# Kernel optimization log

Measured on AMD Instinct MI355X. Metric: run time of the kernel, lower is better.

Reference implementation:

```python
import jax, jax.numpy as jnp
import numpy as np

# EntNet entity-memory update (Henaff et al. 2017), per selected entity i:
#   g_i      = sigmoid(s . h_i + s . w_i)                       (gate)
#   h~_i     = relu(h_i @ U^T + w_i @ V^T + s @ W^T)            (candidate)
#   h_i      = l2_normalize(h_i + g_i * h~_i)
# The original TF code loops over `indices` in Python; since each index touches a
# distinct entity slot, the updates are independent and we vectorize with a single
# gather over the entity axis and a scatter (.at[].set) back.

def setup_inputs() -> dict:
    key = jax.random.key(0)
    ks = jax.random.split(key, 6)
    B, N, D, K = 32, 1024, 1024, 512
    return {
        "encoded_sents": jax.random.normal(ks[0], (B, D), jnp.float32),
        "hiddens": jax.random.normal(ks[1], (B, N, D), jnp.float32),
        "keys": jax.random.normal(ks[2], (B, N, D), jnp.float32),
        "U": jax.random.normal(ks[3], (D, D), jnp.float32),
        "V": jax.random.normal(ks[4], (D, D), jnp.float32),
        "W": jax.random.normal(ks[5], (D, D), jnp.float32),
        "indices": jnp.arange(K, dtype=jnp.int64),
    }

def reference(encoded_sents, hiddens, keys, U, V, W, indices):
    EPS = 1e-12
    h = hiddens[:, indices, :]                     # [B,K,D] gather selected entities
    w = keys[:, indices, :]                        # [B,K,D]
    s = encoded_sents                              # [B,D]
    # gate: sigmoid(s.h_i + s.w_i) -> [B,K]
    g = jax.nn.sigmoid(jnp.einsum('bd,bkd->bk', s, h + w))
    # candidate: relu(h U^T + w V^T + s W^T) -> [B,K,D]
    h_tilde = jax.nn.relu(
        jnp.einsum('bkd,ed->bke', h, U)
        + jnp.einsum('bkd,ed->bke', w, V)
        + (s @ W.T)[:, None, :]
    )
    h_new = h + g[..., None] * h_tilde
    # tf.math.l2_normalize: x * rsqrt(max(sum(x^2), eps))
    h_new = h_new * jax.lax.rsqrt(jnp.maximum(jnp.sum(h_new * h_new, axis=-1, keepdims=True), EPS))
    # scatter updated entities back
    return hiddens.at[:, indices, :].set(h_new)
```

## Files before the change

kernel.cpp:

```cpp
#include <hip/hip_runtime.h>

constexpr int Bb = 32;
constexpr int Nn = 1024;
constexpr int Dd = 1024;
constexpr int Kk = 512;
constexpr int Mm = Bb * Kk;
constexpr int KD = 2 * Dd;

using bf16x8 = __bf16 __attribute__((ext_vector_type(8)));
using f32x4  = float __attribute__((ext_vector_type(4)));

constexpr size_t WS_ABF  = 0;
constexpr size_t WS_BBF  = (size_t)Mm * KD * 2;
constexpr size_t WS_G    = WS_BBF + (size_t)Nn * KD * 2;
constexpr size_t WS_SW   = WS_G + Mm * sizeof(float);
constexpr size_t WS_RN   = WS_SW + Bb * Nn * sizeof(float);
constexpr size_t WS_MASK = WS_RN + Mm * sizeof(float);

__global__ void mask_kernel(const int* __restrict__ idx, int* __restrict__ mask) {
  int t = threadIdx.x;
  mask[t] = 0;
  __syncthreads();
  if (t < Kk) mask[idx[t]] = 1;
}

__global__ void copy_kernel(const float* __restrict__ hiddens,
                            const int* __restrict__ mask,
                            float* __restrict__ out) {
  int bid = blockIdx.x;
  int n = bid & (Nn - 1);
  if (mask[n]) return;
  size_t base = (size_t)bid * Dd + threadIdx.x * 4;
  *(f32x4*)(out + base) = *(const f32x4*)(hiddens + base);
}

__global__ void prep_b_kernel(const float* __restrict__ U,
                              const float* __restrict__ V,
                              __bf16* __restrict__ Bbf) {
  int t = blockIdx.x * 256 + threadIdx.x;
  int e = t >> 8;
  int c = (t & 255) << 3;
  const float* src = (c < Dd) ? (U + (size_t)e * Dd + c)
                              : (V + (size_t)e * Dd + (c - Dd));
  f32x4 f0 = *(const f32x4*)src;
  f32x4 f1 = *(const f32x4*)(src + 4);
  bf16x8 v;
  v[0] = (__bf16)f0[0]; v[1] = (__bf16)f0[1]; v[2] = (__bf16)f0[2]; v[3] = (__bf16)f0[3];
  v[4] = (__bf16)f1[0]; v[5] = (__bf16)f1[1]; v[6] = (__bf16)f1[2]; v[7] = (__bf16)f1[3];
  *(bf16x8*)(Bbf + (size_t)e * KD + c) = v;
}

__global__ void sw_kernel(const float* __restrict__ s,
                          const float* __restrict__ W,
                          float* __restrict__ sW) {
  int e = blockIdx.x * 4 + (threadIdx.x >> 6);
  int lane = threadIdx.x & 63;
  const float* wp = W + (size_t)e * Dd;
  float wr[16];
#pragma unroll
  for (int c = 0; c < 4; c++) {
    f32x4 wv = *(const f32x4*)(wp + c * 256 + lane * 4);
    wr[c*4+0] = wv[0]; wr[c*4+1] = wv[1]; wr[c*4+2] = wv[2]; wr[c*4+3] = wv[3];
  }
  for (int b = 0; b < Bb; b++) {
    const float* sp = s + (size_t)b * Dd;
    float acc = 0.f;
#pragma unroll
    for (int c = 0; c < 4; c++) {
      f32x4 sv = *(const f32x4*)(sp + c * 256 + lane * 4);
      acc += sv[0]*wr[c*4+0] + sv[1]*wr[c*4+1] + sv[2]*wr[c*4+2] + sv[3]*wr[c*4+3];
    }
#pragma unroll
    for (int off = 32; off; off >>= 1) acc += __shfl_xor(acc, off);
    if (lane == 0) sW[b * Nn + e] = acc;
  }
}

__global__ void pack_g_kernel(const float* __restrict__ s,
                              const float* __restrict__ hiddens,
                              const float* __restrict__ keys,
                              const int* __restrict__ idx,
                              __bf16* __restrict__ Abf,
                              float* __restrict__ g) {
  int m = blockIdx.x * 4 + (threadIdx.x >> 6);
  int lane = threadIdx.x & 63;
  int b = m >> 9;
  int k = m & (Kk - 1);
  int row = idx[k];
  const float* hp = hiddens + ((size_t)(b * Nn + row)) * Dd;
  const float* wp = keys    + ((size_t)(b * Nn + row)) * Dd;
  const float* sp = s + (size_t)b * Dd;
  __bf16* ap = Abf + (size_t)m * KD;

  float acc = 0.f;
#pragma unroll
  for (int c = 0; c < 2; c++) {
    int d = c * 512 + lane * 8;
    f32x4 h0 = *(const f32x4*)(hp + d);
    f32x4 h1 = *(const f32x4*)(hp + d + 4);
    f32x4 w0 = *(const f32x4*)(wp + d);
    f32x4 w1 = *(const f32x4*)(wp + d + 4);
    f32x4 s0 = *(const f32x4*)(sp + d);
    f32x4 s1 = *(const f32x4*)(sp + d + 4);
    acc += s0[0]*(h0[0]+w0[0]) + s0[1]*(h0[1]+w0[1])
         + s0[2]*(h0[2]+w0[2]) + s0[3]*(h0[3]+w0[3])
         + s1[0]*(h1[0]+w1[0]) + s1[1]*(h1[1]+w1[1])
         + s1[2]*(h1[2]+w1[2]) + s1[3]*(h1[3]+w1[3]);
    bf16x8 hv, wv;
    hv[0]=(__bf16)h0[0]; hv[1]=(__bf16)h0[1]; hv[2]=(__bf16)h0[2]; hv[3]=(__bf16)h0[3];
    hv[4]=(__bf16)h1[0]; hv[5]=(__bf16)h1[1]; hv[6]=(__bf16)h1[2]; hv[7]=(__bf16)h1[3];
    wv[0]=(__bf16)w0[0]; wv[1]=(__bf16)w0[1]; wv[2]=(__bf16)w0[2]; wv[3]=(__bf16)w0[3];
    wv[4]=(__bf16)w1[0]; wv[5]=(__bf16)w1[1]; wv[6]=(__bf16)w1[2]; wv[7]=(__bf16)w1[3];
    *(bf16x8*)(ap + d) = hv;
    *(bf16x8*)(ap + Dd + d) = wv;
  }
#pragma unroll
  for (int off = 32; off; off >>= 1) acc += __shfl_xor(acc, off);
  if (lane == 0) g[m] = 1.f / (1.f + expf(-acc));
}

__global__ __launch_bounds__(256)
void gemm_kernel(const __bf16* __restrict__ Abf,
                 const __bf16* __restrict__ Bbf,
                 const int* __restrict__ idx,
                 const float* __restrict__ sW,
                 const float* __restrict__ g,
                 const float* __restrict__ hiddens,
                 float* __restrict__ rownorm,
                 float* __restrict__ out) {
  __shared__ __bf16 a_lds[128 * 64];
  __shared__ __bf16 b_lds[128 * 64];

  int bid = blockIdx.x;
  int mt = bid & 127;
  int nt = bid >> 7;
  int m0 = mt * 128, e0 = nt * 128;
  int tid = threadIdx.x, lane = tid & 63, wave = tid >> 6;

  int lofs[4]; size_t aoff[4], boff[4];
#pragma unroll
  for (int i = 0; i < 4; i++) {
    int o = (wave * 4 + i) * 1024 + lane * 16;
    lofs[i] = o;
    int row = o >> 7;
    int colb = o & 127;
    aoff[i] = ((size_t)(m0 + row) * KD) * 2 + colb;
    boff[i] = ((size_t)(e0 + row) * KD) * 2 + colb;
  }

  f32x4 acc[4][4] = {};
  int wm = (wave >> 1) * 64, we = (wave & 1) * 64;
  int lr = lane & 15, lg = lane >> 4;
  const char* Ab = (const char*)Abf;
  const char* Bbp = (const char*)Bbf;

  for (int t = 0; t < KD / 64; ++t) {
    size_t kb = (size_t)t * 128;
#pragma unroll
    for (int i = 0; i < 4; i++) {
      __builtin_amdgcn_global_load_lds(
          (const __attribute__((address_space(1))) void*)(Ab + aoff[i] + kb),
          (__attribute__((address_space(3))) void*)((char*)a_lds + lofs[i]),
          16, 0, 0);
      __builtin_amdgcn_global_load_lds(
          (const __attribute__((address_space(1))) void*)(Bbp + boff[i] + kb),
          (__attribute__((address_space(3))) void*)((char*)b_lds + lofs[i]),
          16, 0, 0);
    }
    __syncthreads();

#pragma unroll
    for (int kh = 0; kh < 2; ++kh) {
      bf16x8 af[4], bfr[4];
#pragma unroll
      for (int i = 0; i < 4; i++)
        af[i] = *(const bf16x8*)&a_lds[(wm + i * 16 + lr) * 64 + kh * 32 + lg * 8];
#pragma unroll
      for (int j = 0; j < 4; j++)
        bfr[j] = *(const bf16x8*)&b_lds[(we + j * 16 + lr) * 64 + kh * 32 + lg * 8];
#pragma unroll
      for (int i = 0; i < 4; i++)
#pragma unroll
        for (int j = 0; j < 4; j++)
          acc[i][j] = __builtin_amdgcn_mfma_f32_16x16x32_bf16(af[i], bfr[j], acc[i][j], 0, 0, 0);
    }
    __syncthreads();
  }

#pragma unroll
  for (int i = 0; i < 4; i++) {
#pragma unroll
    for (int r = 0; r < 4; r++) {
      int m = m0 + wm + i * 16 + lg * 4 + r;
      int b = m >> 9;
      int rowidx = idx[m & (Kk - 1)];
      size_t base = ((size_t)(b * Nn + rowidx)) * Dd;
      float gg = g[m];
      float part = 0.f;
#pragma unroll
      for (int j = 0; j < 4; j++) {
        int e = e0 + we + j * 16 + lr;
        float ht = acc[i][j][r] + sW[b * Nn + e];
        ht = fmaxf(ht, 0.f);
        float v = hiddens[base + e] + gg * ht;
        out[base + e] = v;
        part += v * v;
      }
      part += __shfl_xor(part, 1);
      part += __shfl_xor(part, 2);
      part += __shfl_xor(part, 4);
      part += __shfl_xor(part, 8);
      if (lr == 0) atomicAdd(&rownorm[m], part);
    }
  }
}

__global__ void norm_kernel(const int* __restrict__ idx,
                            const float* __restrict__ rownorm,
                            float* __restrict__ out) {
  int m = blockIdx.x;
  int b = m >> 9;
  int rowidx = idx[m & (Kk - 1)];
  float nr = fmaxf(rownorm[m], 1e-12f);
  float y = rsqrtf(nr);
  y = y * (1.5f - 0.5f * nr * y * y);
  f32x4* p = (f32x4*)(out + ((size_t)(b * Nn + rowidx)) * Dd);
  f32x4 v = p[threadIdx.x];
  v[0] *= y; v[1] *= y; v[2] *= y; v[3] *= y;
  p[threadIdx.x] = v;
}

extern "C" void kernel_launch(void* const* d_in, const int* in_sizes, int n_in,
                              void* d_out, int out_size, void* d_ws, size_t ws_size,
                              hipStream_t stream) {
  const float* s       = (const float*)d_in[0];
  const float* hiddens = (const float*)d_in[1];
  const float* keys    = (const float*)d_in[2];
  const float* U       = (const float*)d_in[3];
  const float* V       = (const float*)d_in[4];
  const float* W       = (const float*)d_in[5];
  const int*   idx     = (const int*)d_in[6];
  float* out = (float*)d_out;

  char* ws = (char*)d_ws;
  __bf16* Abf   = (__bf16*)(ws + WS_ABF);
  __bf16* Bbf   = (__bf16*)(ws + WS_BBF);
  float*  g     = (float*)(ws + WS_G);
  float*  sW    = (float*)(ws + WS_SW);
  float*  rnorm = (float*)(ws + WS_RN);
  int*    mask  = (int*)(ws + WS_MASK);

  hipMemsetAsync(rnorm, 0, Mm * sizeof(float), stream);
  mask_kernel<<<1, Nn, 0, stream>>>(idx, mask);
  copy_kernel<<<Bb * Nn, 256, 0, stream>>>(hiddens, mask, out);
  prep_b_kernel<<<1024, 256, 0, stream>>>(U, V, Bbf);
  sw_kernel<<<Nn / 4, 256, 0, stream>>>(s, W, sW);
  pack_g_kernel<<<Mm / 4, 256, 0, stream>>>(s, hiddens, keys, idx, Abf, g);
  gemm_kernel<<<(Mm / 128) * (Nn / 128), 256, 0, stream>>>(
      Abf, Bbf, idx, sW, g, hiddens, rnorm, out);
  norm_kernel<<<Mm, 256, 0, stream>>>(idx, rnorm, out);
}
```

Before: 519.4 us.

## Fuse copy with row packing and rewrite GEMM as double-buffered 256x256 tiles

The separate copy and pack kernels are merged into one per-row kernel. Each block either copies an unselected hidden row or converts a selected row to bf16 and computes its gate, and the mask now stores the slot index. The GEMM is restructured to 256x256 tiles with 512 threads and a double-buffered LDS of 128 KB. It uses XOR-swizzled LDS addressing, staged half-tile async loads interleaved with MFMA phases, and s_setprio around the math. This aims to overlap global loads with compute, cut LDS bank conflicts and remove a launch, at the cost of much higher LDS use and more complex, fragile synchronisation.

Result: faster. 486.2 us (-6.4%).

```diff
diff --git a/kernel.cpp b/kernel.cpp
--- a/kernel.cpp
+++ b/kernel.cpp
@@ -6,6 +6,7 @@
 constexpr int Kk = 512;
 constexpr int Mm = Bb * Kk;
 constexpr int KD = 2 * Dd;
+constexpr int NT = KD / 64;
 
 using bf16x8 = __bf16 __attribute__((ext_vector_type(8)));
 using f32x4  = float __attribute__((ext_vector_type(4)));
@@ -21,17 +22,7 @@
   int t = threadIdx.x;
   mask[t] = 0;
   __syncthreads();
-  if (t < Kk) mask[idx[t]] = 1;
-}
-
-__global__ void copy_kernel(const float* __restrict__ hiddens,
-                            const int* __restrict__ mask,
-                            float* __restrict__ out) {
-  int bid = blockIdx.x;
-  int n = bid & (Nn - 1);
-  if (mask[n]) return;
-  size_t base = (size_t)bid * Dd + threadIdx.x * 4;
-  *(f32x4*)(out + base) = *(const f32x4*)(hiddens + base);
+  if (t < Kk) mask[idx[t]] = t + 1;
 }
 
 __global__ void prep_b_kernel(const float* __restrict__ U,
@@ -45,8 +36,8 @@
   f32x4 f0 = *(const f32x4*)src;
   f32x4 f1 = *(const f32x4*)(src + 4);
   bf16x8 v;
-  v[0] = (__bf16)f0[0]; v[1] = (__bf16)f0[1]; v[2] = (__bf16)f0[2]; v[3] = (__bf16)f0[3];
-  v[4] = (__bf16)f1[0]; v[5] = (__bf16)f1[1]; v[6] = (__bf16)f1[2]; v[7] = (__bf16)f1[3];
+  v[0]=(__bf16)f0[0]; v[1]=(__bf16)f0[1]; v[2]=(__bf16)f0[2]; v[3]=(__bf16)f0[3];
+  v[4]=(__bf16)f1[0]; v[5]=(__bf16)f1[1]; v[6]=(__bf16)f1[2]; v[7]=(__bf16)f1[3];
   *(bf16x8*)(Bbf + (size_t)e * KD + c) = v;
 }
 
@@ -60,7 +51,7 @@
 #pragma unroll
   for (int c = 0; c < 4; c++) {
     f32x4 wv = *(const f32x4*)(wp + c * 256 + lane * 4);
-    wr[c*4+0] = wv[0]; wr[c*4+1] = wv[1]; wr[c*4+2] = wv[2]; wr[c*4+3] = wv[3];
+    wr[c*4+0]=wv[0]; wr[c*4+1]=wv[1]; wr[c*4+2]=wv[2]; wr[c*4+3]=wv[3];
   }
   for (int b = 0; b < Bb; b++) {
     const float* sp = s + (size_t)b * Dd;
@@ -76,50 +67,93 @@
   }
 }
 
-__global__ void pack_g_kernel(const float* __restrict__ s,
-                              const float* __restrict__ hiddens,
-                              const float* __restrict__ keys,
-                              const int* __restrict__ idx,
-                              __bf16* __restrict__ Abf,
-                              float* __restrict__ g) {
-  int m = blockIdx.x * 4 + (threadIdx.x >> 6);
-  int lane = threadIdx.x & 63;
-  int b = m >> 9;
-  int k = m & (Kk - 1);
-  int row = idx[k];
-  const float* hp = hiddens + ((size_t)(b * Nn + row)) * Dd;
-  const float* wp = keys    + ((size_t)(b * Nn + row)) * Dd;
-  const float* sp = s + (size_t)b * Dd;
-  __bf16* ap = Abf + (size_t)m * KD;
-
-  float acc = 0.f;
-#pragma unroll
-  for (int c = 0; c < 2; c++) {
-    int d = c * 512 + lane * 8;
-    f32x4 h0 = *(const f32x4*)(hp + d);
-    f32x4 h1 = *(const f32x4*)(hp + d + 4);
-    f32x4 w0 = *(const f32x4*)(wp + d);
-    f32x4 w1 = *(const f32x4*)(wp + d + 4);
-    f32x4 s0 = *(const f32x4*)(sp + d);
-    f32x4 s1 = *(const f32x4*)(sp + d + 4);
-    acc += s0[0]*(h0[0]+w0[0]) + s0[1]*(h0[1]+w0[1])
-         + s0[2]*(h0[2]+w0[2]) + s0[3]*(h0[3]+w0[3])
-         + s1[0]*(h1[0]+w1[0]) + s1[1]*(h1[1]+w1[1])
-         + s1[2]*(h1[2]+w1[2]) + s1[3]*(h1[3]+w1[3]);
-    bf16x8 hv, wv;
-    hv[0]=(__bf16)h0[0]; hv[1]=(__bf16)h0[1]; hv[2]=(__bf16)h0[2]; hv[3]=(__bf16)h0[3];
-    hv[4]=(__bf16)h1[0]; hv[5]=(__bf16)h1[1]; hv[6]=(__bf16)h1[2]; hv[7]=(__bf16)h1[3];
-    wv[0]=(__bf16)w0[0]; wv[1]=(__bf16)w0[1]; wv[2]=(__bf16)w0[2]; wv[3]=(__bf16)w0[3];
-    wv[4]=(__bf16)w1[0]; wv[5]=(__bf16)w1[1]; wv[6]=(__bf16)w1[2]; wv[7]=(__bf16)w1[3];
-    *(bf16x8*)(ap + d) = hv;
-    *(bf16x8*)(ap + Dd + d) = wv;
-  }
-#pragma unroll
-  for (int off = 32; off; off >>= 1) acc += __shfl_xor(acc, off);
-  if (lane == 0) g[m] = 1.f / (1.f + expf(-acc));
-}
-
 __global__ __launch_bounds__(256)
+void prep_rows_kernel(const float* __restrict__ s,
+                      const float* __restrict__ hiddens,
+                      const float* __restrict__ keys,
+                      const int* __restrict__ mask,
+                      __bf16* __restrict__ Abf,
+                      float* __restrict__ g_out,
+                      float* __restrict__ out) {
+  __shared__ float red[4];
+  int bid = blockIdx.x;
+  int b = bid >> 10, n = bid & 1023;
+  int tid = threadIdx.x;
+  int mk = mask[n];
+  const float* hp = hiddens + (size_t)bid * Dd;
+  if (mk == 0) {
+    ((f32x4*)(out + (size_t)bid * Dd))[tid] = ((const f32x4*)hp)[tid];
+    return;
+  }
+  int m = b * Kk + (mk - 1);
+  const float* src = (tid < 128) ? hp : (keys + (size_t)bid * Dd);
+  int d = (tid & 127) * 8;
+  const float* sp = s + (size_t)b * Dd + d;
+  f32x4 x0 = *(const f32x4*)(src + d);
+  f32x4 x1 = *(const f32x4*)(src + d + 4);
+  f32x4 s0 = *(const f32x4*)sp;
+  f32x4 s1 = *(const f32x4*)(sp + 4);
+  float part = s0[0]*x0[0]+s0[1]*x0[1]+s0[2]*x0[2]+s0[3]*x0[3]
+             + s1[0]*x1[0]+s1[1]*x1[1]+s1[2]*x1[2]+s1[3]*x1[3];
+  bf16x8 v;
+  v[0]=(__bf16)x0[0]; v[1]=(__bf16)x0[1]; v[2]=(__bf16)x0[2]; v[3]=(__bf16)x0[3];
+  v[4]=(__bf16)x1[0]; v[5]=(__bf16)x1[1]; v[6]=(__bf16)x1[2]; v[7]=(__bf16)x1[3];
+  *(bf16x8*)(Abf + (size_t)m * KD + (tid < 128 ? 0 : Dd) + d) = v;
+#pragma unroll
+  for (int off = 32; off; off >>= 1) part += __shfl_xor(part, off);
+  if ((tid & 63) == 0) red[tid >> 6] = part;
+  __syncthreads();
+  if (tid == 0) {
+    float acc = red[0] + red[1] + red[2] + red[3];
+    g_out[m] = 1.f / (1.f + expf(-acc));
+  }
+}
+
+#define VMW(N) asm volatile("s_waitcnt vmcnt(" #N ")" ::: "memory")
+#define BAR()  __builtin_amdgcn_s_barrier()
+#define PRI1() __builtin_amdgcn_s_setprio(1)
+#define PRI0() __builtin_amdgcn_s_setprio(0)
+
+#define STAGE_HALF(SRC, LDSOFF, BUF, HALF, KT)                                  \
+  { _Pragma("unroll")                                                           \
+    for (int i_ = 0; i_ < 2; ++i_) {                                            \
+      __builtin_amdgcn_global_load_lds(                                         \
+        (const __attribute__((address_space(1))) void*)                         \
+            ((SRC) + (size_t)((HALF)*128 + i_*64)*4096 + (size_t)(KT)*128),     \
+        (__attribute__((address_space(3))) void*)                               \
+            (ldsc + (LDSOFF) + (BUF)*32768 + (HALF)*16384 + i_*8192 + t16),     \
+        16, 0, 0);                                                              \
+    } }
+
+#define LDA4(D, BUF, RBASE)                                                     \
+  { _Pragma("unroll")                                                           \
+    for (int i_ = 0; i_ < 4; ++i_) {                                            \
+      const char* p_ = ldsc + (BUF)*32768 + ((RBASE) + i_*16 + lr)*128;         \
+      D[i_][0] = *(const bf16x8*)(p_ + kb0);                                    \
+      D[i_][1] = *(const bf16x8*)(p_ + kb1);                                    \
+    } }
+
+#define LDB2(D, BUF, RBASE)                                                     \
+  { _Pragma("unroll")                                                           \
+    for (int j_ = 0; j_ < 2; ++j_) {                                            \
+      const char* p_ = ldsc + 65536 + (BUF)*32768 + ((RBASE) + j_*16 + lr)*128; \
+      D[j_][0] = *(const bf16x8*)(p_ + kb0);                                    \
+      D[j_][1] = *(const bf16x8*)(p_ + kb1);                                    \
+    } }
+
+#define MF16(IOFF, JOFF, AF, BF)                                                \
+  { _Pragma("unroll")                                                           \
+    for (int i_ = 0; i_ < 4; ++i_)                                              \
+      { _Pragma("unroll")                                                       \
+        for (int j_ = 0; j_ < 2; ++j_)                                          \
+          { _Pragma("unroll")                                                   \
+            for (int k_ = 0; k_ < 2; ++k_)                                      \
+              acc[(IOFF)+i_][(JOFF)+j_] =                                       \
+                __builtin_amdgcn_mfma_f32_16x16x32_bf16(                        \
+                  AF[i_][k_], BF[j_][k_], acc[(IOFF)+i_][(JOFF)+j_], 0, 0, 0);  \
+          } } }
+
+__global__ __launch_bounds__(512, 2)
 void gemm_kernel(const __bf16* __restrict__ Abf,
                  const __bf16* __restrict__ Bbf,
                  const int* __restrict__ idx,
@@ -128,78 +162,79 @@
                  const float* __restrict__ hiddens,
                  float* __restrict__ rownorm,
                  float* __restrict__ out) {
-  __shared__ __bf16 a_lds[128 * 64];
-  __shared__ __bf16 b_lds[128 * 64];
-
-  int bid = blockIdx.x;
-  int mt = bid & 127;
-  int nt = bid >> 7;
-  int m0 = mt * 128, e0 = nt * 128;
-  int tid = threadIdx.x, lane = tid & 63, wave = tid >> 6;
-
-  int lofs[4]; size_t aoff[4], boff[4];
-#pragma unroll
-  for (int i = 0; i < 4; i++) {
-    int o = (wave * 4 + i) * 1024 + lane * 16;
-    lofs[i] = o;
-    int row = o >> 7;
-    int colb = o & 127;
-    aoff[i] = ((size_t)(m0 + row) * KD) * 2 + colb;
-    boff[i] = ((size_t)(e0 + row) * KD) * 2 + colb;
-  }
-
-  f32x4 acc[4][4] = {};
-  int wm = (wave >> 1) * 64, we = (wave & 1) * 64;
-  int lr = lane & 15, lg = lane >> 4;
-  const char* Ab = (const char*)Abf;
-  const char* Bbp = (const char*)Bbf;
-
-  for (int t = 0; t < KD / 64; ++t) {
-    size_t kb = (size_t)t * 128;
-#pragma unroll
-    for (int i = 0; i < 4; i++) {
-      __builtin_amdgcn_global_load_lds(
-          (const __attribute__((address_space(1))) void*)(Ab + aoff[i] + kb),
-          (__attribute__((address_space(3))) void*)((char*)a_lds + lofs[i]),
-          16, 0, 0);
-      __builtin_amdgcn_global_load_lds(
-          (const __attribute__((address_space(1))) void*)(Bbp + boff[i] + kb),
-          (__attribute__((address_space(3))) void*)((char*)b_lds + lofs[i]),
-          16, 0, 0);
-    }
-    __syncthreads();
-
-#pragma unroll
-    for (int kh = 0; kh < 2; ++kh) {
-      bf16x8 af[4], bfr[4];
-#pragma unroll
-      for (int i = 0; i < 4; i++)
-        af[i] = *(const bf16x8*)&a_lds[(wm + i * 16 + lr) * 64 + kh * 32 + lg * 8];
-#pragma unroll
-      for (int j = 0; j < 4; j++)
-        bfr[j] = *(const bf16x8*)&b_lds[(we + j * 16 + lr) * 64 + kh * 32 + lg * 8];
-#pragma unroll
-      for (int i = 0; i < 4; i++)
-#pragma unroll
-        for (int j = 0; j < 4; j++)
-          acc[i][j] = __builtin_amdgcn_mfma_f32_16x16x32_bf16(af[i], bfr[j], acc[i][j], 0, 0, 0);
-    }
-    __syncthreads();
-  }
-
-#pragma unroll
-  for (int i = 0; i < 4; i++) {
-#pragma unroll
-    for (int r = 0; r < 4; r++) {
-      int m = m0 + wm + i * 16 + lg * 4 + r;
+  __shared__ __bf16 lds[65536];
+  char* ldsc = (char*)lds;
+
+  const int bid = blockIdx.x;
+  const int mt = bid >> 2, nt = bid & 3;
+  const int m0 = mt * 256, e0 = nt * 256;
+  const int tid = threadIdx.x;
+  const int lane = tid & 63, wid = tid >> 6;
+  const int wr = wid >> 2, wc = wid & 3;
+  const int lr = lane & 15, lg = lane >> 4;
+
+  const int t16  = tid * 16;
+  const int colb = t16 & 127;
+  const int r_lo = t16 >> 7;
+  const int scol = colb ^ ((r_lo & 7) << 4);
+  const char* Asrc = (const char*)Abf + (size_t)(m0 + r_lo) * 4096 + scol;
+  const char* Bsrc = (const char*)Bbf + (size_t)(e0 + r_lo) * 4096 + scol;
+
+  const int key = (lr & 7) << 4;
+  const int kb0 = (lg * 16) ^ key;
+  const int kb1 = (64 + lg * 16) ^ key;
+
+  f32x4 acc[8][4] = {};
+  bf16x8 aLo[4][2], aHi[4][2], bLo[2][2], bHi[2][2];
+
+  STAGE_HALF(Asrc, 0,     0, 0, 0);
+  STAGE_HALF(Bsrc, 65536, 0, 0, 0);
+  STAGE_HALF(Asrc, 0,     0, 1, 0);
+  STAGE_HALF(Bsrc, 65536, 0, 1, 0);
+  VMW(4);
+  BAR();
+
+  for (int n = 0; n < NT - 1; ++n) {
+    const int buf = n & 1, sbuf = buf ^ 1;
+    LDA4(aLo, buf, wr * 64);
+    LDB2(bLo, buf, wc * 32);
+    STAGE_HALF(Asrc, 0, sbuf, 0, n + 1);
+    VMW(4); BAR(); PRI1(); MF16(0, 0, aLo, bLo); PRI0(); BAR();
+    LDA4(aHi, buf, wr * 64 + 128);
+    STAGE_HALF(Bsrc, 65536, sbuf, 0, n + 1);
+    VMW(4); BAR(); PRI1(); MF16(4, 0, aHi, bLo); PRI0(); BAR();
+    LDB2(bHi, buf, wc * 32 + 128);
+    STAGE_HALF(Asrc, 0, sbuf, 1, n + 1);
+    VMW(4); BAR(); PRI1(); MF16(0, 2, aLo, bHi); PRI0(); BAR();
+    STAGE_HALF(Bsrc, 65536, sbuf, 1, n + 1);
+    VMW(4); BAR(); PRI1(); MF16(4, 2, aHi, bHi); PRI0(); BAR();
+  }
+  {
+    const int buf = (NT - 1) & 1;
+    LDA4(aLo, buf, wr * 64);
+    LDB2(bLo, buf, wc * 32);
+    VMW(2); BAR(); PRI1(); MF16(0, 0, aLo, bLo); PRI0(); BAR();
+    LDA4(aHi, buf, wr * 64 + 128);
+    VMW(0); BAR(); PRI1(); MF16(4, 0, aHi, bLo); PRI0(); BAR();
+    LDB2(bHi, buf, wc * 32 + 128);
+    BAR(); PRI1(); MF16(0, 2, aLo, bHi); PRI0(); BAR();
+    PRI1(); MF16(4, 2, aHi, bHi); PRI0();
+  }
+
+#pragma unroll
+  for (int i = 0; i < 8; ++i) {
+    const int mrow = m0 + (i & 3) * 16 + wr * 64 + (i >> 2) * 128;
+#pragma unroll
+    for (int r = 0; r < 4; ++r) {
+      int m = mrow + lg * 4 + r;
       int b = m >> 9;
       int rowidx = idx[m & (Kk - 1)];
       size_t base = ((size_t)(b * Nn + rowidx)) * Dd;
       float gg = g[m];
       float part = 0.f;
 #pragma unroll
-      for (int j = 0; j < 4; j++) {
-        int e = e0 + we + j * 16 + lr;
+      for (int j = 0; j < 4; ++j) {
+        int e = e0 + (j & 1) * 16 + wc * 32 + (j >> 1) * 128 + lr;
         float ht = acc[i][j][r] + sW[b * Nn + e];
         ht = fmaxf(ht, 0.f);
         float v = hiddens[base + e] + gg * ht;
@@ -252,11 +287,10 @@
 
   hipMemsetAsync(rnorm, 0, Mm * sizeof(float), stream);
   mask_kernel<<<1, Nn, 0, stream>>>(idx, mask);
-  copy_kernel<<<Bb * Nn, 256, 0, stream>>>(hiddens, mask, out);
   prep_b_kernel<<<1024, 256, 0, stream>>>(U, V, Bbf);
   sw_kernel<<<Nn / 4, 256, 0, stream>>>(s, W, sW);
-  pack_g_kernel<<<Mm / 4, 256, 0, stream>>>(s, hiddens, keys, idx, Abf, g);
-  gemm_kernel<<<(Mm / 128) * (Nn / 128), 256, 0, stream>>>(
+  prep_rows_kernel<<<Bb * Nn, 256, 0, stream>>>(s, hiddens, keys, mask, Abf, g, out);
+  gemm_kernel<<<(Mm / 256) * (Nn / 256), 512, 0, stream>>>(
       Abf, Bbf, idx, sW, g, hiddens, rnorm, out);
   norm_kernel<<<Mm, 256, 0, stream>>>(idx, rnorm, out);
 }
```
